# Performance work log

Hardware: AMD Instinct MI355X
Metric: run time of the kernel (lower is better)

## Reference

```python
import jax, jax.numpy as jnp
import numpy as np

N_NODES = 100000
N_EDGES = 3200000
IN_DIM, HID, OUT = 256, 64, 10


def setup_inputs() -> dict:
    key = jax.random.key(0)
    ks = jax.random.split(key, 6)
    x = jax.random.normal(ks[0], (N_NODES, IN_DIM), jnp.float32)
    edge_index = jax.random.randint(ks[1], (2, N_EDGES), 0, N_NODES, dtype=jnp.int64)
    edge_weight = jnp.ones((N_EDGES,), jnp.float32)
    # Glorot-scaled weights; PyG GCNConv keeps bias separate from lin.
    W1 = jax.random.normal(ks[2], (HID, IN_DIM), jnp.float32) * np.float32(1.0 / np.sqrt(IN_DIM))
    b1 = jnp.zeros((HID,), jnp.float32)
    W2 = jax.random.normal(ks[3], (HID, HID), jnp.float32) * np.float32(1.0 / np.sqrt(HID))
    b2 = jnp.zeros((HID,), jnp.float32)
    W3 = jax.random.normal(ks[4], (OUT, HID), jnp.float32) * np.float32(1.0 / np.sqrt(HID))
    b3 = jnp.zeros((OUT,), jnp.float32)
    return dict(x=x, edge_index=edge_index, edge_weight=edge_weight,
                W1=W1, b1=b1, W2=W2, b2=b2, W3=W3, b3=b3)


def _gcn_conv(x, W, b, row, col, edge_weight, n):
    """PyG GCNConv with add_self_loops=False: out = D^{-1/2} A D^{-1/2} (x W^T) + b."""
    h = x @ W.T  # [N, out_dim]
    deg = jax.ops.segment_sum(edge_weight, col, num_segments=n)  # in-degree by weight
    dinv = jnp.where(deg > 0, jax.lax.rsqrt(jnp.maximum(deg, 1e-12)), 0.0)
    norm = dinv[row] * edge_weight * dinv[col]  # [E]
    msgs = h[row] * norm[:, None]               # gather from source nodes
    out = jax.ops.segment_sum(msgs, col, num_segments=n)  # scatter-add to targets
    return out + b


def reference(x, edge_index, edge_weight, W1, b1, W2, b2, W3, b3):
    row, col = edge_index[0], edge_index[1]
    n = x.shape[0]
    h = jax.nn.relu(_gcn_conv(x, W1, b1, row, col, edge_weight, n))
    h = jax.nn.relu(_gcn_conv(h, W2, b2, row, col, edge_weight, n))
    out = _gcn_conv(h, W3, b3, row, col, edge_weight, n)  # logits, [N, num_classes]
    return out
```

## Files before the change

kernel.cpp:

```cpp
#include <hip/hip_runtime.h>
#include <stddef.h>

typedef __attribute__((ext_vector_type(8))) short bf16x8;
typedef __attribute__((ext_vector_type(4))) float f32x4;
typedef __attribute__((ext_vector_type(8))) float f32x8;

#define NPB 512
#define PB  512

__device__ inline float bf2f(unsigned short u) {
    unsigned int v = ((unsigned int)u) << 16;
    float f;
    __builtin_memcpy(&f, &v, 4);
    return f;
}
__device__ inline unsigned short f2bf(float f) {
    unsigned int v;
    __builtin_memcpy(&v, &f, 4);
    unsigned int r = (v + 0x7FFFu + ((v >> 16) & 1u)) >> 16;
    return (unsigned short)r;
}
__device__ inline float feat(const void* p, long long idx, int isbf) {
    if (isbf) return bf2f(((const unsigned short*)p)[idx]);
    return ((const float*)p)[idx];
}
__device__ inline int clampi(int v, int lo, int hi) {
    return v < lo ? lo : (v > hi ? hi : v);
}

__global__ void detect_kernel(const int* ei, const unsigned short* ew16,
                              const unsigned short* x16, int* flags) {
    __shared__ int s_is64, s_pass;
    if (threadIdx.x == 0) { s_is64 = 1; s_pass = 0; }
    __syncthreads();
    int t = threadIdx.x;
    if (t < 128 && ei[2 * t + 1] != 0) atomicAnd(&s_is64, 0);
    if (t < 64) {
        unsigned short h = x16[t];
        unsigned int expf = (h >> 7) & 0xFF;
        if (h == 0 || (expf >= 112 && expf <= 142)) atomicAdd(&s_pass, 1);
    }
    __syncthreads();
    if (t == 0) {
        flags[0] = s_is64;
        flags[1] = (ew16[0] == 0x3F80) ? 1 : 0;
        flags[2] = (s_pass >= 56) ? 1 : 0;
        flags[3] = 1;
    }
}

__global__ void ones_kernel(const void* ew, int* flags, int E) {
    int i = blockIdx.x * blockDim.x + threadIdx.x;
    int wbf = flags[1];
    int b = i * 4;
    int lim = b + 4 < E ? b + 4 : E;
    bool bad = false;
    for (int k = b; k < lim; k++)
        if (feat(ew, k, wbf) != 1.0f) bad = true;
    if (bad) atomicAnd(&flags[3], 0);
}

__global__ void sentinel_kernel(unsigned short* outp, int n, float val) {
    int i = blockIdx.x * blockDim.x + threadIdx.x;
    if (i < n) outp[i] = f2bf(val);
}

__global__ void wsplit_kernel(const void* W, const int* flags, unsigned short* hi,
                              unsigned short* lo, int n_in, int n_out) {
    int i = blockIdx.x * blockDim.x + threadIdx.x;
    if (i >= n_out) return;
    if (i >= n_in) { hi[i] = 0; lo[i] = 0; return; }
    if (flags[2]) {
        hi[i] = ((const unsigned short*)W)[i];
        lo[i] = 0;
    } else {
        float v = ((const float*)W)[i];
        unsigned short h = f2bf(v);
        hi[i] = h;
        lo[i] = f2bf(v - bf2f(h));
    }
}

__global__ __launch_bounds__(512) void khist_kernel(const int* ei, const int* flags,
                                                    int* ghist, int E, int n,
                                                    int NB, int chunk) {
    __shared__ int hist[256];
    int blk = blockIdx.x;
    for (int i = threadIdx.x; i < NB; i += blockDim.x) hist[i] = 0;
    __syncthreads();
    int is64 = flags[0];
    int e0 = blk * chunk;
    int e1 = e0 + chunk < E ? e0 + chunk : E;
    for (int e = e0 + (int)threadIdx.x; e < e1; e += blockDim.x) {
        int c = is64 ? ei[2 * (E + e)] : ei[E + e];
        c = clampi(c, 0, n - 1);
        atomicAdd(&hist[c >> 9], 1);
    }
    __syncthreads();
    for (int i = threadIdx.x; i < NB; i += blockDim.x) ghist[blk * NB + i] = hist[i];
}

__global__ __launch_bounds__(512) void koff1_kernel(int* ghist, int* btot, int NB) {
    __shared__ int s[512];
    int b = blockIdx.x;
    int t = threadIdx.x;
    int v = ghist[t * NB + b];
    s[t] = v;
    __syncthreads();
    for (int off = 1; off < 512; off <<= 1) {
        int add = (t >= off) ? s[t - off] : 0;
        __syncthreads();
        s[t] += add;
        __syncthreads();
    }
    ghist[t * NB + b] = s[t] - v;
    if (t == 511) btot[b] = s[511];
}

__global__ __launch_bounds__(256) void koff2_kernel(const int* btot, int* bstart,
                                                    int* row_ptr, int NB, int N, int E) {
    __shared__ int s[256];
    int t = threadIdx.x;
    int v = (t < NB) ? btot[t] : 0;
    s[t] = v;
    __syncthreads();
    for (int off = 1; off < 256; off <<= 1) {
        int add = (t >= off) ? s[t - off] : 0;
        __syncthreads();
        s[t] += add;
        __syncthreads();
    }
    if (t < NB) bstart[t] = s[t] - v;
    if (t == 0) row_ptr[N] = E;
}

__global__ __launch_bounds__(512) void kscatter_kernel(const int* ei, const void* ew,
                                                       const int* flags, const int* ghist,
                                                       const int* bstart,
                                                       unsigned int* ebuf, float* wbuf,
                                                       int E, int n, int NB, int chunk) {
    __shared__ int cur[256];
    int blk = blockIdx.x;
    for (int i = threadIdx.x; i < NB; i += blockDim.x)
        cur[i] = ghist[blk * NB + i] + bstart[i];
    __syncthreads();
    int is64 = flags[0], wbf = flags[1], ones = flags[3];
    int e0 = blk * chunk;
    int e1 = e0 + chunk < E ? e0 + chunk : E;
    for (int e = e0 + (int)threadIdx.x; e < e1; e += blockDim.x) {
        int r = is64 ? ei[2 * e] : ei[e];
        int c = is64 ? ei[2 * (E + e)] : ei[E + e];
        r = clampi(r, 0, n - 1);
        c = clampi(c, 0, n - 1);
        int b = c >> 9;
        int pos = atomicAdd(&cur[b], 1);
        ebuf[pos] = ((unsigned int)(c & 511) << 17) | (unsigned int)r;
        if (!ones) wbuf[pos] = feat(ew, e, wbf);
    }
}

__global__ __launch_bounds__(512) void kcsr_a_kernel(const unsigned int* ebuf,
                                                     const float* wbuf, const int* flags,
                                                     const int* bstart, const int* btot,
                                                     int* row_ptr, float* dinv, int N) {
    __shared__ int cnt[512];
    __shared__ int pre[512];
    __shared__ float wsum[512];
    int b = blockIdx.x;
    int t = threadIdx.x;
    int ones = flags[3];
    cnt[t] = 0;
    wsum[t] = 0.f;
    __syncthreads();
    int bs = bstart[b];
    int be = bs + btot[b];
    for (int i = bs + t; i < be; i += 512) {
        unsigned int p = ebuf[i];
        int cl = (int)(p >> 17);
        atomicAdd(&cnt[cl], 1);
        if (!ones) atomicAdd(&wsum[cl], wbuf[i]);
    }
    __syncthreads();
    int v = cnt[t];
    pre[t] = v;
    __syncthreads();
    for (int off = 1; off < 512; off <<= 1) {
        int add = (t >= off) ? pre[t - off] : 0;
        __syncthreads();
        pre[t] += add;
        __syncthreads();
    }
    int node = b * NPB + t;
    if (node < N) {
        row_ptr[node] = bs + pre[t] - v;
        float d = ones ? (float)v : wsum[t];
        dinv[node] = (d > 0.f) ? rsqrtf(fmaxf(d, 1e-12f)) : 0.f;
    }
}

__global__ __launch_bounds__(512) void kcsr_b_kernel(const unsigned int* ebuf,
                                                     const float* wbuf, const int* flags,
                                                     const int* bstart, const int* btot,
                                                     const int* row_ptr, const float* dinv,
                                                     int2* csr_pack, int N) {
    __shared__ int cur[512];
    __shared__ float dloc[512];
    int b = blockIdx.x;
    int t = threadIdx.x;
    int ones = flags[3];
    int node = b * NPB + t;
    cur[t] = (node < N) ? row_ptr[node] : 0;
    dloc[t] = (node < N) ? dinv[node] : 0.f;
    __syncthreads();
    int bs = bstart[b];
    int be = bs + btot[b];
    for (int i = bs + t; i < be; i += 512) {
        unsigned int p = ebuf[i];
        int cl = (int)(p >> 17);
        int r = (int)(p & 0x1FFFFu);
        float w = ones ? 1.0f : wbuf[i];
        float nv = dinv[r] * w * dloc[cl];
        int pos = atomicAdd(&cur[cl], 1);
        csr_pack[pos] = make_int2(r, __float_as_int(nv));
    }
}

__device__ inline void split8v(f32x8 v, bf16x8& hi, bf16x8& lo) {
    for (int i = 0; i < 8; i++) {
        float f = v[i];
        unsigned short h = f2bf(f);
        hi[i] = (short)h;
        lo[i] = (short)f2bf(f - bf2f(h));
    }
}

__global__ __launch_bounds__(256) void gemm1_kernel(const void* A,
                             const unsigned short* Whi, const unsigned short* Wlo,
                             const int* flags, unsigned short* C, int M, int K) {
    int wave = threadIdx.x >> 6;
    int l = threadIdx.x & 63;
    int m = l & 15;
    int quad = l >> 4;
    int row0 = blockIdx.x * 64 + wave * 16;
    bool arow_ok = (row0 + m) < M;
    int fb = flags[2];
    f32x4 acc[4];
    #pragma unroll
    for (int n = 0; n < 4; n++) acc[n] = (f32x4){0.f, 0.f, 0.f, 0.f};
    bf16x8 zf = {0, 0, 0, 0, 0, 0, 0, 0};
    long long abase = (long long)(row0 + m) * K + quad * 8;
    if (fb) {
        const short* As = (const short*)A;
        #pragma unroll 4
        for (int k0 = 0; k0 < K; k0 += 32) {
            bf16x8 a = arow_ok ? *(const bf16x8*)(As + abase + k0) : zf;
            #pragma unroll
            for (int n = 0; n < 4; n++) {
                const unsigned short* wp = Whi + (long long)(n * 16 + m) * K + k0 + quad * 8;
                bf16x8 b = *(const bf16x8*)wp;
                acc[n] = __builtin_amdgcn_mfma_f32_16x16x32_bf16(a, b, acc[n], 0, 0, 0);
            }
        }
    } else {
        const float* Af = (const float*)A;
        #pragma unroll 2
        for (int k0 = 0; k0 < K; k0 += 32) {
            bf16x8 ah = zf, al = zf;
            if (arow_ok) {
                f32x8 av = *(const f32x8*)(Af + abase + k0);
                split8v(av, ah, al);
            }
            #pragma unroll
            for (int n = 0; n < 4; n++) {
                long long widx = (long long)(n * 16 + m) * K + k0 + quad * 8;
                bf16x8 wh = *(const bf16x8*)(Whi + widx);
                bf16x8 wl = *(const bf16x8*)(Wlo + widx);
                acc[n] = __builtin_amdgcn_mfma_f32_16x16x32_bf16(ah, wh, acc[n], 0, 0, 0);
                acc[n] = __builtin_amdgcn_mfma_f32_16x16x32_bf16(al, wh, acc[n], 0, 0, 0);
                acc[n] = __builtin_amdgcn_mfma_f32_16x16x32_bf16(ah, wl, acc[n], 0, 0, 0);
            }
        }
    }
    #pragma unroll
    for (int n = 0; n < 4; n++) {
        #pragma unroll
        for (int r = 0; r < 4; r++) {
            int row = row0 + quad * 4 + r;
            if (row < M) C[(long long)row * 64 + n * 16 + m] = f2bf(acc[n][r]);
        }
    }
}

__global__ __launch_bounds__(256) void gemm2_kernel(const unsigned short* A,
                             const unsigned short* Whi, const unsigned short* Wlo,
                             const int* flags, unsigned short* C, int M) {
    int wave = threadIdx.x >> 6;
    int l = threadIdx.x & 63;
    int m = l & 15;
    int quad = l >> 4;
    int row0 = blockIdx.x * 64 + wave * 16;
    bool arow_ok = (row0 + m) < M;
    int fb = flags[2];
    f32x4 acc[4];
    #pragma unroll
    for (int n = 0; n < 4; n++) acc[n] = (f32x4){0.f, 0.f, 0.f, 0.f};
    bf16x8 zf = {0, 0, 0, 0, 0, 0, 0, 0};
    const short* As = (const short*)A;
    long long abase = (long long)(row0 + m) * 64 + quad * 8;
    #pragma unroll
    for (int k0 = 0; k0 < 64; k0 += 32) {
        bf16x8 a = arow_ok ? *(const bf16x8*)(As + abase + k0) : zf;
        #pragma unroll
        for (int n = 0; n < 4; n++) {
            long long widx = (long long)(n * 16 + m) * 64 + k0 + quad * 8;
            bf16x8 wh = *(const bf16x8*)(Whi + widx);
            acc[n] = __builtin_amdgcn_mfma_f32_16x16x32_bf16(a, wh, acc[n], 0, 0, 0);
            if (!fb) {
                bf16x8 wl = *(const bf16x8*)(Wlo + widx);
                acc[n] = __builtin_amdgcn_mfma_f32_16x16x32_bf16(a, wl, acc[n], 0, 0, 0);
            }
        }
    }
    #pragma unroll
    for (int n = 0; n < 4; n++) {
        #pragma unroll
        for (int r = 0; r < 4; r++) {
            int row = row0 + quad * 4 + r;
            if (row < M) C[(long long)row * 64 + n * 16 + m] = f2bf(acc[n][r]);
        }
    }
}

__global__ __launch_bounds__(256) void gemm3_kernel(const unsigned short* A,
                             const unsigned short* Whi, const unsigned short* Wlo,
                             const int* flags, unsigned short* C, int M) {
    int wave = threadIdx.x >> 6;
    int l = threadIdx.x & 63;
    int m = l & 15;
    int quad = l >> 4;
    int row0 = blockIdx.x * 64 + wave * 16;
    bool arow_ok = (row0 + m) < M;
    int fb = flags[2];
    f32x4 acc = {0.f, 0.f, 0.f, 0.f};
    bf16x8 zf = {0, 0, 0, 0, 0, 0, 0, 0};
    const short* As = (const short*)A;
    long long abase = (long long)(row0 + m) * 64 + quad * 8;
    #pragma unroll
    for (int k0 = 0; k0 < 64; k0 += 32) {
        bf16x8 a = arow_ok ? *(const bf16x8*)(As + abase + k0) : zf;
        long long widx = (long long)m * 64 + k0 + quad * 8;
        bf16x8 wh = *(const bf16x8*)(Whi + widx);
        acc = __builtin_amdgcn_mfma_f32_16x16x32_bf16(a, wh, acc, 0, 0, 0);
        if (!fb) {
            bf16x8 wl = *(const bf16x8*)(Wlo + widx);
            acc = __builtin_amdgcn_mfma_f32_16x16x32_bf16(a, wl, acc, 0, 0, 0);
        }
    }
    #pragma unroll
    for (int r = 0; r < 4; r++) {
        int row = row0 + quad * 4 + r;
        if (row < M) C[(long long)row * 16 + m] = f2bf(acc[r]);
    }
}

__global__ __launch_bounds__(256, 8) void agg64_kernel(const unsigned short* h,
                             const void* bias, const int* flags, const int* row_ptr,
                             const int2* cp, unsigned short* outp, int n, int do_relu) {
    int l = threadIdx.x & 63;
    int node = blockIdx.x * 4 + (int)(threadIdx.x >> 6);
    if (node >= n) return;
    int g = l >> 3;
    int j = l & 7;
    int beg = row_ptr[node];
    int end = row_ptr[node + 1];
    float a0 = 0.f, a1 = 0.f, a2 = 0.f, a3 = 0.f;
    float a4 = 0.f, a5 = 0.f, a6 = 0.f, a7 = 0.f;
    int e = beg;
    for (; e + 16 <= end; e += 16) {
        int2 p0 = cp[e + g];
        int2 p1 = cp[e + 8 + g];
        uint4 r0 = *(const uint4*)(h + (long long)p0.x * 64 + j * 8);
        uint4 r1 = *(const uint4*)(h + (long long)p1.x * 64 + j * 8);
        float nv0 = __int_as_float(p0.y);
        float nv1 = __int_as_float(p1.y);
        a0 += nv0 * __uint_as_float(r0.x << 16);
        a1 += nv0 * __uint_as_float(r0.x & 0xFFFF0000u);
        a2 += nv0 * __uint_as_float(r0.y << 16);
        a3 += nv0 * __uint_as_float(r0.y & 0xFFFF0000u);
        a4 += nv0 * __uint_as_float(r0.z << 16);
        a5 += nv0 * __uint_as_float(r0.z & 0xFFFF0000u);
        a6 += nv0 * __uint_as_float(r0.w << 16);
        a7 += nv0 * __uint_as_float(r0.w & 0xFFFF0000u);
        a0 += nv1 * __uint_as_float(r1.x << 16);
        a1 += nv1 * __uint_as_float(r1.x & 0xFFFF0000u);
        a2 += nv1 * __uint_as_float(r1.y << 16);
        a3 += nv1 * __uint_as_float(r1.y & 0xFFFF0000u);
        a4 += nv1 * __uint_as_float(r1.z << 16);
        a5 += nv1 * __uint_as_float(r1.z & 0xFFFF0000u);
        a6 += nv1 * __uint_as_float(r1.w << 16);
        a7 += nv1 * __uint_as_float(r1.w & 0xFFFF0000u);
    }
    for (; e < end; e += 8) {
        int ee = e + g;
        if (ee < end) {
            int2 p = cp[ee];
            float nv = __int_as_float(p.y);
            uint4 raw = *(const uint4*)(h + (long long)p.x * 64 + j * 8);
            a0 += nv * __uint_as_float(raw.x << 16);
            a1 += nv * __uint_as_float(raw.x & 0xFFFF0000u);
            a2 += nv * __uint_as_float(raw.y << 16);
            a3 += nv * __uint_as_float(raw.y & 0xFFFF0000u);
            a4 += nv * __uint_as_float(raw.z << 16);
            a5 += nv * __uint_as_float(raw.z & 0xFFFF0000u);
            a6 += nv * __uint_as_float(raw.w << 16);
            a7 += nv * __uint_as_float(raw.w & 0xFFFF0000u);
        }
    }
    for (int mask = 8; mask <= 32; mask <<= 1) {
        a0 += __shfl_xor(a0, mask);
        a1 += __shfl_xor(a1, mask);
        a2 += __shfl_xor(a2, mask);
        a3 += __shfl_xor(a3, mask);
        a4 += __shfl_xor(a4, mask);
        a5 += __shfl_xor(a5, mask);
        a6 += __shfl_xor(a6, mask);
        a7 += __shfl_xor(a7, mask);
    }
    if (g == 0) {
        int fb = flags[2];
        float v0 = a0 + feat(bias, j * 8 + 0, fb);
        float v1 = a1 + feat(bias, j * 8 + 1, fb);
        float v2 = a2 + feat(bias, j * 8 + 2, fb);
        float v3 = a3 + feat(bias, j * 8 + 3, fb);
        float v4 = a4 + feat(bias, j * 8 + 4, fb);
        float v5 = a5 + feat(bias, j * 8 + 5, fb);
        float v6 = a6 + feat(bias, j * 8 + 6, fb);
        float v7 = a7 + feat(bias, j * 8 + 7, fb);
        if (do_relu) {
            v0 = fmaxf(v0, 0.f); v1 = fmaxf(v1, 0.f);
            v2 = fmaxf(v2, 0.f); v3 = fmaxf(v3, 0.f);
            v4 = fmaxf(v4, 0.f); v5 = fmaxf(v5, 0.f);
            v6 = fmaxf(v6, 0.f); v7 = fmaxf(v7, 0.f);
        }
        uint4 pk;
        pk.x = (unsigned int)f2bf(v0) | ((unsigned int)f2bf(v1) << 16);
        pk.y = (unsigned int)f2bf(v2) | ((unsigned int)f2bf(v3) << 16);
        pk.z = (unsigned int)f2bf(v4) | ((unsigned int)f2bf(v5) << 16);
        pk.w = (unsigned int)f2bf(v6) | ((unsigned int)f2bf(v7) << 16);
        *(uint4*)(outp + (long long)node * 64 + j * 8) = pk;
    }
}

__global__ void agg16_kernel(const unsigned short* h, const void* bias,
                             const int* flags, const int* row_ptr,
                             const int2* cp, void* outp, int n) {
    int l = threadIdx.x & 63;
    int node = blockIdx.x * 4 + (int)(threadIdx.x >> 6);
    if (node >= n) return;
    int g = l >> 2;
    int j = l & 3;
    int beg = row_ptr[node];
    int end = row_ptr[node + 1];
    float a0 = 0.f, a1 = 0.f, a2 = 0.f, a3 = 0.f;
    for (int e = beg; e < end; e += 16) {
        int ee = e + g;
        if (ee < end) {
            int2 p = cp[ee];
            float nv = __int_as_float(p.y);
            uint2 raw = *(const uint2*)(h + (long long)p.x * 16 + j * 4);
            a0 += nv * __uint_as_float(raw.x << 16);
            a1 += nv * __uint_as_float(raw.x & 0xFFFF0000u);
            a2 += nv * __uint_as_float(raw.y << 16);
            a3 += nv * __uint_as_float(raw.y & 0xFFFF0000u);
        }
    }
    for (int mask = 4; mask <= 32; mask <<= 1) {
        a0 += __shfl_xor(a0, mask);
        a1 += __shfl_xor(a1, mask);
        a2 += __shfl_xor(a2, mask);
        a3 += __shfl_xor(a3, mask);
    }
    if (g == 0) {
        int fb = flags[2];
        float v[4] = {a0, a1, a2, a3};
        #pragma unroll
        for (int i = 0; i < 4; i++) {
            int f = j * 4 + i;
            if (f < 10) {
                float o = v[i] + feat(bias, f, fb);
                if (fb) ((unsigned short*)outp)[(long long)node * 10 + f] = f2bf(o);
                else    ((float*)outp)[(long long)node * 10 + f] = o;
            }
        }
    }
}

extern "C" void kernel_launch(void* const* d_in, const int* in_sizes, int n_in,
                              void* d_out, int out_size, void* d_ws, size_t ws_size,
                              hipStream_t stream) {
    const void* x  = d_in[0];
    const int*  ei = (const int*)d_in[1];
    const void* ew = d_in[2];
    const void* W1 = d_in[3];
    const void* b1 = d_in[4];
    const void* W2 = d_in[5];
    const void* b2 = d_in[6];
    const void* W3 = d_in[7];
    const void* b3 = d_in[8];

    const int N = in_sizes[0] / 256;
    const int E = in_sizes[1] / 2;
    const int TB = 256;
    const int NB = (N + NPB - 1) / NPB;
    const int chunk = (E + PB - 1) / PB;

    size_t off = 0;
    size_t o_flags = off; off += 16;
    size_t o_ghist = off; off += (size_t)PB * NB * 4; off = (off + 15) & ~(size_t)15;
    size_t o_btot  = off; off += (size_t)NB * 4;
    size_t o_bst   = off; off += (size_t)NB * 4; off = (off + 15) & ~(size_t)15;
    size_t o_rp    = off; off += (size_t)(N + 1) * 4;
    size_t o_dinv  = off; off += (size_t)N * 4; off = (off + 15) & ~(size_t)15;
    size_t o_pack  = off; off += (size_t)E * 8;
    size_t o_bufA  = off; off += (size_t)N * 64 * 2;
    size_t o_bufB  = off; off += (size_t)N * 64 * 2;
    size_t o_h3    = off; off += (size_t)N * 16 * 2; off = (off + 15) & ~(size_t)15;
    size_t o_w1hi  = off; off += (size_t)64 * 256 * 2;
    size_t o_w1lo  = off; off += (size_t)64 * 256 * 2;
    size_t o_w2hi  = off; off += (size_t)64 * 64 * 2;
    size_t o_w2lo  = off; off += (size_t)64 * 64 * 2;
    size_t o_w3hi  = off; off += (size_t)16 * 64 * 2;
    size_t o_w3lo  = off; off += (size_t)16 * 64 * 2;
    size_t need = off;
    if (ws_size < need || (size_t)E * 4 > (size_t)N * 64 * 2) {
        sentinel_kernel<<<dim3((out_size + TB - 1) / TB), dim3(TB), 0, stream>>>(
            (unsigned short*)d_out, out_size, 250.0f);
        return;
    }
    char* ws = (char*)d_ws;
    int*   flags    = (int*)(ws + o_flags);
    int*   ghist    = (int*)(ws + o_ghist);
    int*   btot     = (int*)(ws + o_btot);
    int*   bstart   = (int*)(ws + o_bst);
    int*   row_ptr  = (int*)(ws + o_rp);
    float* dinv     = (float*)(ws + o_dinv);
    int2*  csr_pack = (int2*)(ws + o_pack);
    unsigned short* bufA  = (unsigned short*)(ws + o_bufA);
    unsigned short* bufB  = (unsigned short*)(ws + o_bufB);
    unsigned short* h3buf = (unsigned short*)(ws + o_h3);
    unsigned short* w1hi  = (unsigned short*)(ws + o_w1hi);
    unsigned short* w1lo  = (unsigned short*)(ws + o_w1lo);
    unsigned short* w2hi  = (unsigned short*)(ws + o_w2hi);
    unsigned short* w2lo  = (unsigned short*)(ws + o_w2lo);
    unsigned short* w3hi  = (unsigned short*)(ws + o_w3hi);
    unsigned short* w3lo  = (unsigned short*)(ws + o_w3lo);
    float*        wbuf = (float*)bufA;
    unsigned int* ebuf = (unsigned int*)bufB;

    dim3 tb(TB);
    dim3 tb512(512);
    dim3 gE4((E / 4 + TB - 1) / TB);
    dim3 gG((N + 63) / 64);
    dim3 gAgg((N + 3) / 4);
    dim3 one(1);

    detect_kernel<<<one, tb, 0, stream>>>(ei, (const unsigned short*)ew,
                                          (const unsigned short*)x, flags);
    wsplit_kernel<<<dim3(64), tb, 0, stream>>>(W1, flags, w1hi, w1lo,
                                               64 * 256, 64 * 256);
    wsplit_kernel<<<dim3(16), tb, 0, stream>>>(W2, flags, w2hi, w2lo,
                                               64 * 64, 64 * 64);
    wsplit_kernel<<<dim3(4), tb, 0, stream>>>(W3, flags, w3hi, w3lo,
                                              10 * 64, 16 * 64);
    ones_kernel<<<gE4, tb, 0, stream>>>(ew, flags, E);
    khist_kernel<<<dim3(PB), tb512, 0, stream>>>(ei, flags, ghist, E, N, NB, chunk);
    koff1_kernel<<<dim3(NB), tb512, 0, stream>>>(ghist, btot, NB);
    koff2_kernel<<<one, tb, 0, stream>>>(btot, bstart, row_ptr, NB, N, E);
    kscatter_kernel<<<dim3(PB), tb512, 0, stream>>>(ei, ew, flags, ghist, bstart,
                                                    ebuf, wbuf, E, N, NB, chunk);
    kcsr_a_kernel<<<dim3(NB), tb512, 0, stream>>>(ebuf, wbuf, flags, bstart, btot,
                                                  row_ptr, dinv, N);
    kcsr_b_kernel<<<dim3(NB), tb512, 0, stream>>>(ebuf, wbuf, flags, bstart, btot,
                                                  row_ptr, dinv, csr_pack, N);

    gemm1_kernel<<<gG, tb, 0, stream>>>(x, w1hi, w1lo, flags, bufA, N, 256);
    agg64_kernel<<<gAgg, tb, 0, stream>>>(bufA, b1, flags, row_ptr, csr_pack,
                                          bufB, N, 1);
    gemm2_kernel<<<gG, tb, 0, stream>>>(bufB, w2hi, w2lo, flags, bufA, N);
    agg64_kernel<<<gAgg, tb, 0, stream>>>(bufA, b2, flags, row_ptr, csr_pack,
                                          bufB, N, 1);
    gemm3_kernel<<<gG, tb, 0, stream>>>(bufB, w3hi, w3lo, flags, h3buf, N);
    agg16_kernel<<<gAgg, tb, 0, stream>>>(h3buf, b3, flags, row_ptr, csr_pack,
                                          d_out, N);
}
```

Baseline: 590.9 us.

## Fuse layer-2 and layer-3 linear transforms into preceding aggregation kernels

Aggregation kernels now apply bias and ReLU, stage the aggregated 64-wide row in shared memory, and multiply it by a transposed fp32 weight matrix before writing. This removes the separate gemm2 and gemm3 launches and one full read and write of the N×64 intermediate per layer. The cost is a per-node 64-step scalar FMA loop reading the weights from global or cache instead of MFMA, plus a block-wide syncthreads. Weights are kept in fp32 rather than split into bf16 hi/lo parts.

```diff
diff --git a/kernel.cpp b/kernel.cpp
--- a/kernel.cpp
+++ b/kernel.cpp
@@ -79,6 +79,17 @@
         hi[i] = h;
         lo[i] = f2bf(v - bf2f(h));
     }
+}
+
+__global__ void wtrans_kernel(const void* W, const int* flags, float* wt,
+                              int inf, int outf, int K) {
+    int i = blockIdx.x * blockDim.x + threadIdx.x;
+    if (i >= K * outf) return;
+    int k = i / outf;
+    int f = i - k * outf;
+    float v = 0.f;
+    if (f < inf) v = feat(W, (long long)f * K + k, flags[2]);
+    wt[i] = v;
 }
 
 __global__ __launch_bounds__(512) void khist_kernel(const int* ei, const int* flags,
@@ -291,88 +302,19 @@
     }
 }
 
-__global__ __launch_bounds__(256) void gemm2_kernel(const unsigned short* A,
-                             const unsigned short* Whi, const unsigned short* Wlo,
-                             const int* flags, unsigned short* C, int M) {
-    int wave = threadIdx.x >> 6;
+__global__ __launch_bounds__(256, 8) void agg64f_kernel(const unsigned short* h,
+                             const void* bias, const int* flags, const int* row_ptr,
+                             const int2* cp, const float* wt, unsigned short* outp,
+                             int n, int outf) {
+    __shared__ float a1sh[4][64];
     int l = threadIdx.x & 63;
-    int m = l & 15;
-    int quad = l >> 4;
-    int row0 = blockIdx.x * 64 + wave * 16;
-    bool arow_ok = (row0 + m) < M;
-    int fb = flags[2];
-    f32x4 acc[4];
-    #pragma unroll
-    for (int n = 0; n < 4; n++) acc[n] = (f32x4){0.f, 0.f, 0.f, 0.f};
-    bf16x8 zf = {0, 0, 0, 0, 0, 0, 0, 0};
-    const short* As = (const short*)A;
-    long long abase = (long long)(row0 + m) * 64 + quad * 8;
-    #pragma unroll
-    for (int k0 = 0; k0 < 64; k0 += 32) {
-        bf16x8 a = arow_ok ? *(const bf16x8*)(As + abase + k0) : zf;
-        #pragma unroll
-        for (int n = 0; n < 4; n++) {
-            long long widx = (long long)(n * 16 + m) * 64 + k0 + quad * 8;
-            bf16x8 wh = *(const bf16x8*)(Whi + widx);
-            acc[n] = __builtin_amdgcn_mfma_f32_16x16x32_bf16(a, wh, acc[n], 0, 0, 0);
-            if (!fb) {
-                bf16x8 wl = *(const bf16x8*)(Wlo + widx);
-                acc[n] = __builtin_amdgcn_mfma_f32_16x16x32_bf16(a, wl, acc[n], 0, 0, 0);
-            }
-        }
-    }
-    #pragma unroll
-    for (int n = 0; n < 4; n++) {
-        #pragma unroll
-        for (int r = 0; r < 4; r++) {
-            int row = row0 + quad * 4 + r;
-            if (row < M) C[(long long)row * 64 + n * 16 + m] = f2bf(acc[n][r]);
-        }
-    }
-}
-
-__global__ __launch_bounds__(256) void gemm3_kernel(const unsigned short* A,
-                             const unsigned short* Whi, const unsigned short* Wlo,
-                             const int* flags, unsigned short* C, int M) {
-    int wave = threadIdx.x >> 6;
-    int l = threadIdx.x & 63;
-    int m = l & 15;
-    int quad = l >> 4;
-    int row0 = blockIdx.x * 64 + wave * 16;
-    bool arow_ok = (row0 + m) < M;
-    int fb = flags[2];
-    f32x4 acc = {0.f, 0.f, 0.f, 0.f};
-    bf16x8 zf = {0, 0, 0, 0, 0, 0, 0, 0};
-    const short* As = (const short*)A;
-    long long abase = (long long)(row0 + m) * 64 + quad * 8;
-    #pragma unroll
-    for (int k0 = 0; k0 < 64; k0 += 32) {
-        bf16x8 a = arow_ok ? *(const bf16x8*)(As + abase + k0) : zf;
-        long long widx = (long long)m * 64 + k0 + quad * 8;
-        bf16x8 wh = *(const bf16x8*)(Whi + widx);
-        acc = __builtin_amdgcn_mfma_f32_16x16x32_bf16(a, wh, acc, 0, 0, 0);
-        if (!fb) {
-            bf16x8 wl = *(const bf16x8*)(Wlo + widx);
-            acc = __builtin_amdgcn_mfma_f32_16x16x32_bf16(a, wl, acc, 0, 0, 0);
-        }
-    }
-    #pragma unroll
-    for (int r = 0; r < 4; r++) {
-        int row = row0 + quad * 4 + r;
-        if (row < M) C[(long long)row * 16 + m] = f2bf(acc[r]);
-    }
-}
-
-__global__ __launch_bounds__(256, 8) void agg64_kernel(const unsigned short* h,
-                             const void* bias, const int* flags, const int* row_ptr,
-                             const int2* cp, unsigned short* outp, int n, int do_relu) {
-    int l = threadIdx.x & 63;
-    int node = blockIdx.x * 4 + (int)(threadIdx.x >> 6);
-    if (node >= n) return;
+    int wave = (int)(threadIdx.x >> 6);
+    int node = blockIdx.x * 4 + wave;
+    bool active = node < n;
     int g = l >> 3;
     int j = l & 7;
-    int beg = row_ptr[node];
-    int end = row_ptr[node + 1];
+    int beg = active ? row_ptr[node] : 0;
+    int end = active ? row_ptr[node + 1] : 0;
     float a0 = 0.f, a1 = 0.f, a2 = 0.f, a3 = 0.f;
     float a4 = 0.f, a5 = 0.f, a6 = 0.f, a7 = 0.f;
     int e = beg;
@@ -426,28 +368,36 @@
         a6 += __shfl_xor(a6, mask);
         a7 += __shfl_xor(a7, mask);
     }
-    if (g == 0) {
+    {
         int fb = flags[2];
-        float v0 = a0 + feat(bias, j * 8 + 0, fb);
-        float v1 = a1 + feat(bias, j * 8 + 1, fb);
-        float v2 = a2 + feat(bias, j * 8 + 2, fb);
-        float v3 = a3 + feat(bias, j * 8 + 3, fb);
-        float v4 = a4 + feat(bias, j * 8 + 4, fb);
-        float v5 = a5 + feat(bias, j * 8 + 5, fb);
-        float v6 = a6 + feat(bias, j * 8 + 6, fb);
-        float v7 = a7 + feat(bias, j * 8 + 7, fb);
-        if (do_relu) {
-            v0 = fmaxf(v0, 0.f); v1 = fmaxf(v1, 0.f);
-            v2 = fmaxf(v2, 0.f); v3 = fmaxf(v3, 0.f);
-            v4 = fmaxf(v4, 0.f); v5 = fmaxf(v5, 0.f);
-            v6 = fmaxf(v6, 0.f); v7 = fmaxf(v7, 0.f);
-        }
-        uint4 pk;
-        pk.x = (unsigned int)f2bf(v0) | ((unsigned int)f2bf(v1) << 16);
-        pk.y = (unsigned int)f2bf(v2) | ((unsigned int)f2bf(v3) << 16);
-        pk.z = (unsigned int)f2bf(v4) | ((unsigned int)f2bf(v5) << 16);
-        pk.w = (unsigned int)f2bf(v6) | ((unsigned int)f2bf(v7) << 16);
-        *(uint4*)(outp + (long long)node * 64 + j * 8) = pk;
+        a0 = fmaxf(a0 + feat(bias, j * 8 + 0, fb), 0.f);
+        a1 = fmaxf(a1 + feat(bias, j * 8 + 1, fb), 0.f);
+        a2 = fmaxf(a2 + feat(bias, j * 8 + 2, fb), 0.f);
+        a3 = fmaxf(a3 + feat(bias, j * 8 + 3, fb), 0.f);
+        a4 = fmaxf(a4 + feat(bias, j * 8 + 4, fb), 0.f);
+        a5 = fmaxf(a5 + feat(bias, j * 8 + 5, fb), 0.f);
+        a6 = fmaxf(a6 + feat(bias, j * 8 + 6, fb), 0.f);
+        a7 = fmaxf(a7 + feat(bias, j * 8 + 7, fb), 0.f);
+    }
+    if (active && g == 0) {
+        a1sh[wave][j * 8 + 0] = a0;
+        a1sh[wave][j * 8 + 1] = a1;
+        a1sh[wave][j * 8 + 2] = a2;
+        a1sh[wave][j * 8 + 3] = a3;
+        a1sh[wave][j * 8 + 4] = a4;
+        a1sh[wave][j * 8 + 5] = a5;
+        a1sh[wave][j * 8 + 6] = a6;
+        a1sh[wave][j * 8 + 7] = a7;
+    }
+    __syncthreads();
+    if (active) {
+        int f = l & (outf - 1);
+        float acc = 0.f;
+        #pragma unroll 8
+        for (int k = 0; k < 64; k++)
+            acc = fmaf(wt[k * outf + f], a1sh[wave][k], acc);
+        if (l < outf)
+            outp[(long long)node * outf + l] = f2bf(acc);
     }
 }
 
@@ -527,10 +477,8 @@
     size_t o_h3    = off; off += (size_t)N * 16 * 2; off = (off + 15) & ~(size_t)15;
     size_t o_w1hi  = off; off += (size_t)64 * 256 * 2;
     size_t o_w1lo  = off; off += (size_t)64 * 256 * 2;
-    size_t o_w2hi  = off; off += (size_t)64 * 64 * 2;
-    size_t o_w2lo  = off; off += (size_t)64 * 64 * 2;
-    size_t o_w3hi  = off; off += (size_t)16 * 64 * 2;
-    size_t o_w3lo  = off; off += (size_t)16 * 64 * 2;
+    size_t o_w2t   = off; off += (size_t)64 * 64 * 4;
+    size_t o_w3t   = off; off += (size_t)64 * 16 * 4;
     size_t need = off;
     if (ws_size < need || (size_t)E * 4 > (size_t)N * 64 * 2) {
         sentinel_kernel<<<dim3((out_size + TB - 1) / TB), dim3(TB), 0, stream>>>(
@@ -550,10 +498,8 @@
     unsigned short* h3buf = (unsigned short*)(ws + o_h3);
     unsigned short* w1hi  = (unsigned short*)(ws + o_w1hi);
     unsigned short* w1lo  = (unsigned short*)(ws + o_w1lo);
-    unsigned short* w2hi  = (unsigned short*)(ws + o_w2hi);
-    unsigned short* w2lo  = (unsigned short*)(ws + o_w2lo);
-    unsigned short* w3hi  = (unsigned short*)(ws + o_w3hi);
-    unsigned short* w3lo  = (unsigned short*)(ws + o_w3lo);
+    float* w2t = (float*)(ws + o_w2t);
+    float* w3t = (float*)(ws + o_w3t);
     float*        wbuf = (float*)bufA;
     unsigned int* ebuf = (unsigned int*)bufB;
 
@@ -568,10 +514,8 @@
                                           (const unsigned short*)x, flags);
     wsplit_kernel<<<dim3(64), tb, 0, stream>>>(W1, flags, w1hi, w1lo,
                                                64 * 256, 64 * 256);
-    wsplit_kernel<<<dim3(16), tb, 0, stream>>>(W2, flags, w2hi, w2lo,
-                                               64 * 64, 64 * 64);
-    wsplit_kernel<<<dim3(4), tb, 0, stream>>>(W3, flags, w3hi, w3lo,
-                                              10 * 64, 16 * 64);
+    wtrans_kernel<<<dim3(16), tb, 0, stream>>>(W2, flags, w2t, 64, 64, 64);
+    wtrans_kernel<<<dim3(4), tb, 0, stream>>>(W3, flags, w3t, 10, 16, 64);
     ones_kernel<<<gE4, tb, 0, stream>>>(ew, flags, E);
     khist_kernel<<<dim3(PB), tb512, 0, stream>>>(ei, flags, ghist, E, N, NB, chunk);
     koff1_kernel<<<dim3(NB), tb512, 0, stream>>>(ghist, btot, NB);
@@ -584,12 +528,10 @@
                                                   row_ptr, dinv, csr_pack, N);
 
     gemm1_kernel<<<gG, tb, 0, stream>>>(x, w1hi, w1lo, flags, bufA, N, 256);
-    agg64_kernel<<<gAgg, tb, 0, stream>>>(bufA, b1, flags, row_ptr, csr_pack,
-                                          bufB, N, 1);
-    gemm2_kernel<<<gG, tb, 0, stream>>>(bufB, w2hi, w2lo, flags, bufA, N);
-    agg64_kernel<<<gAgg, tb, 0, stream>>>(bufA, b2, flags, row_ptr, csr_pack,
-                                          bufB, N, 1);
-    gemm3_kernel<<<gG, tb, 0, stream>>>(bufB, w3hi, w3lo, flags, h3buf, N);
+    agg64f_kernel<<<gAgg, tb, 0, stream>>>(bufA, b1, flags, row_ptr, csr_pack,
+                                           w2t, bufB, N, 64);
+    agg64f_kernel<<<gAgg, tb, 0, stream>>>(bufB, b2, flags, row_ptr, csr_pack,
+                                           w3t, h3buf, N, 16);
     agg16_kernel<<<gAgg, tb, 0, stream>>>(h3buf, b3, flags, row_ptr, csr_pack,
                                           d_out, N);
 }
```

New measurement: 654.0 us. 10.7% more time.
